# Kernel optimization log

Measured on AMD Instinct MI355X. Metric: run time of the kernel, lower is better.

## Reference

```python
import jax, jax.numpy as jnp
import numpy as np

E = 8          # num_local_experts
D = 1024       # hidden_size
F = 4096       # intermediate_size_moe
T = 2048       # tokens (seq_len)
K = 2          # num_experts_per_tok


def setup_inputs() -> dict:
    key = jax.random.key(0)
    k_x, k_r, k_g, k_u, k_d = jax.random.split(key, 5)
    s = lambda fan_in: 1.0 / np.sqrt(fan_in)
    return {
        "x_TD": jax.random.normal(k_x, (T, D), dtype=jnp.float32),
        "w_router_DE": jax.random.normal(k_r, (D, E), dtype=jnp.float32) * s(D),
        "kernel_gating_EDF": jax.random.normal(k_g, (E, D, F), dtype=jnp.float32) * s(D),
        "kernel_up_proj_EDF": jax.random.normal(k_u, (E, D, F), dtype=jnp.float32) * s(D),
        "kernel_down_proj_EFD": jax.random.normal(k_d, (E, F, D), dtype=jnp.float32) * s(F),
    }


def reference(x_TD, w_router_DE, kernel_gating_EDF, kernel_up_proj_EDF, kernel_down_proj_EFD):
    # --- Router: softmax -> top-k -> renormalize ---
    logits_TE = x_TD @ w_router_DE                       # [T, E]
    probs_TE = jax.nn.softmax(logits_TE, axis=-1)
    topk_vals, topk_idx = jax.lax.top_k(probs_TE, K)     # [T, K]
    topk_vals = topk_vals / jnp.sum(topk_vals, axis=-1, keepdims=True)  # renormalize=True
    # Dense combine weights: scatter top-k weights back to [T, E]
    weights_TE = jnp.sum(
        jax.nn.one_hot(topk_idx, E, dtype=x_TD.dtype) * topk_vals[..., None], axis=1
    )

    # --- Dense-mat expert MLP (SwiGLU), all experts for all tokens ---
    gate_TEF = jnp.einsum("td,edf->tef", x_TD, kernel_gating_EDF)
    up_TEF = jnp.einsum("td,edf->tef", x_TD, kernel_up_proj_EDF)
    h_TEF = jax.nn.silu(gate_TEF) * up_TEF

    # Down-project each expert and combine weighted by router
    # (apply_expert_weight_before_computation=False -> weight applied at combine)
    out_TD = jnp.einsum("tef,efd,te->td", h_TEF, kernel_down_proj_EFD, weights_TE)
    return out_TD
```

## Files before the change

### kernel.cpp

```cpp
#include <hip/hip_runtime.h>
#include <hip/hip_bf16.h>
#include <math.h>

#define T_TOK 2048
#define D_DIM 1024
#define F_DIM 4096
#define E_NUM 8
#define MAX_TILES 48

typedef __attribute__((ext_vector_type(8))) short short8;
typedef __attribute__((ext_vector_type(4))) short short4v;
typedef __attribute__((ext_vector_type(4))) float floatx4;

__device__ __forceinline__ short f2bf(float f) {
  union { float f; unsigned u; } v; v.f = f;
  unsigned r = v.u + 0x7fffu + ((v.u >> 16) & 1u);
  return (short)(r >> 16);
}

__device__ __forceinline__ void gld_lds16(const void* g, void* l) {
  __builtin_amdgcn_global_load_lds(
      (const __attribute__((address_space(1))) unsigned int*)g,
      (__attribute__((address_space(3))) unsigned int*)l, 16, 0, 0);
}

__global__ __launch_bounds__(256) void router_kernel(
    const float* __restrict__ x, const float* __restrict__ wr,
    int* __restrict__ counts, int* __restrict__ slot_sid, float* __restrict__ slot_w) {
  int lane = threadIdx.x & 63;
  int wave = threadIdx.x >> 6;
  int t = blockIdx.x * 4 + wave;
  const float* xr = x + (size_t)t * D_DIM;
  float acc[8];
#pragma unroll
  for (int e = 0; e < 8; e++) acc[e] = 0.f;
#pragma unroll
  for (int i = 0; i < 16; i++) {
    int d = i * 64 + lane;
    float xv = xr[d];
    const float* w = wr + d * 8;
    float4 w0 = *(const float4*)(w);
    float4 w1 = *(const float4*)(w + 4);
    acc[0] += xv * w0.x; acc[1] += xv * w0.y;
    acc[2] += xv * w0.z; acc[3] += xv * w0.w;
    acc[4] += xv * w1.x; acc[5] += xv * w1.y;
    acc[6] += xv * w1.z; acc[7] += xv * w1.w;
  }
#pragma unroll
  for (int off = 32; off > 0; off >>= 1) {
#pragma unroll
    for (int e = 0; e < 8; e++) acc[e] += __shfl_xor(acc[e], off, 64);
  }
  if (lane == 0) {
    int e1 = 0; float l1 = acc[0];
#pragma unroll
    for (int e = 1; e < 8; e++) { if (acc[e] > l1) { l1 = acc[e]; e1 = e; } }
    int e2 = -1; float l2 = -3.4e38f;
#pragma unroll
    for (int e = 0; e < 8; e++) { if (e != e1 && acc[e] > l2) { l2 = acc[e]; e2 = e; } }
    float w1 = 1.f / (1.f + __expf(l2 - l1));
    float w2 = 1.f - w1;
    int p1 = atomicAdd(&counts[e1], 1);
    slot_sid[e1 * T_TOK + p1] = 2 * t;
    slot_w[e1 * T_TOK + p1] = w1;
    int p2 = atomicAdd(&counts[e2], 1);
    slot_sid[e2 * T_TOK + p2] = 2 * t + 1;
    slot_w[e2 * T_TOK + p2] = w2;
  }
}

__global__ __launch_bounds__(64) void schedule_kernel(
    const int* __restrict__ counts, int* __restrict__ tiles) {
  if (threadIdx.x == 0) {
    int n = 0;
    for (int e = 0; e < E_NUM; e++) {
      int nt_ = (counts[e] + 127) >> 7;
      for (int m = 0; m < nt_; m++) tiles[n++] = (e << 8) | m;
    }
    for (int i = n; i < MAX_TILES; i++) tiles[i] = -1;
  }
}

__global__ __launch_bounds__(256) void cvt_x_kernel(const float* __restrict__ x,
                                                    short* __restrict__ Xb) {
  int i = blockIdx.x * 256 + threadIdx.x;
  float4 v = ((const float4*)x)[i];
  short4v s;
  s[0] = f2bf(v.x); s[1] = f2bf(v.y); s[2] = f2bf(v.z); s[3] = f2bf(v.w);
  ((short4v*)Xb)[i] = s;
}

__global__ __launch_bounds__(256) void transpose_cvt_kernel(
    const float* __restrict__ src, short* __restrict__ dst, int R, int C) {
  __shared__ short tileT[64 * 128];
  int cb = blockIdx.x * 64, rb = blockIdx.y * 128;
  size_t plane = (size_t)blockIdx.z * R * C;
  src += plane; dst += plane;
  int tid = threadIdx.x;
  int r0 = tid >> 4, c4 = (tid & 15) * 4;
#pragma unroll
  for (int i = 0; i < 8; i++) {
    int r = r0 + i * 16;
    float4 v = *(const float4*)&src[(size_t)(rb + r) * C + cb + c4];
    int rhw = ((r >> 3) << 3);
    int rlo = r & 7;
    tileT[(c4 + 0) * 128 + (((r >> 3) ^ ((c4 + 0) & 15)) << 3) + rlo] = f2bf(v.x);
    tileT[(c4 + 1) * 128 + (((r >> 3) ^ ((c4 + 1) & 15)) << 3) + rlo] = f2bf(v.y);
    tileT[(c4 + 2) * 128 + (((r >> 3) ^ ((c4 + 2) & 15)) << 3) + rlo] = f2bf(v.z);
    tileT[(c4 + 3) * 128 + (((r >> 3) ^ ((c4 + 3) & 15)) << 3) + rlo] = f2bf(v.w);
    (void)rhw;
  }
  __syncthreads();
  int c0 = tid >> 4, rq = tid & 15;
#pragma unroll
  for (int i = 0; i < 4; i++) {
    int c = c0 + i * 16;
    short8 s = *(const short8*)&tileT[c * 128 + ((rq ^ (c & 15)) << 3)];
    *(short8*)&dst[(size_t)(cb + c) * R + rb + rq * 8] = s;
  }
}

__global__ __launch_bounds__(256, 4) void gateup_kernel(
    const short* __restrict__ Xb, const short* __restrict__ WgT, const short* __restrict__ WuT,
    const int* __restrict__ counts, const int* __restrict__ slot_sid,
    const int* __restrict__ tiles, short* __restrict__ H) {
  __shared__ short smem[8192];
  __shared__ int s_sid[128];

  int bid = blockIdx.x;
  int tile = tiles[bid >> 6];
  if (tile < 0) return;
  int e  = tile >> 8;
  int mt = tile & 255;
  int nt = bid & 63;
  int n_e = counts[e];

  int tid = threadIdx.x;
  if (tid < 128) {
    int i = mt * 128 + tid;
    if (i > n_e - 1) i = n_e - 1;
    s_sid[tid] = slot_sid[e * T_TOK + i];
  }
  __syncthreads();

  int lane = tid & 63;
  int w = tid >> 6;
  int wm = w >> 1, wn = w & 1;
  int r16 = lane & 15, q = lane >> 4;

  int rl = lane >> 2;
  int kc = (lane & 3) * 8;
  const short* aP0 = Xb + (size_t)(s_sid[w * 16 + rl] >> 1) * D_DIM + kc;
  const short* aP1 = Xb + (size_t)(s_sid[64 + w * 16 + rl] >> 1) * D_DIM + kc;
  size_t wbase = (size_t)e * F_DIM * D_DIM + (size_t)(nt * 64 + w * 16 + rl) * D_DIM;
  const short* gP = WgT + wbase + kc;
  const short* uP = WuT + wbase + kc;
  short* ldsA0 = smem + w * 512;
  short* ldsA1 = smem + 2048 + w * 512;
  short* ldsBg = smem + 4096 + w * 512;
  short* ldsBu = smem + 6144 + w * 512;

  floatx4 zero4 = {0.f, 0.f, 0.f, 0.f};
  floatx4 accg[4][2], accu[4][2];
#pragma unroll
  for (int a = 0; a < 4; a++)
#pragma unroll
    for (int b = 0; b < 2; b++) { accg[a][b] = zero4; accu[a][b] = zero4; }

  for (int kb = 0; kb < D_DIM / 32; kb++) {
    gld_lds16(aP0, ldsA0);
    gld_lds16(aP1, ldsA1);
    gld_lds16(gP, ldsBg);
    gld_lds16(uP, ldsBu);
    aP0 += 32; aP1 += 32; gP += 32; uP += 32;
    __syncthreads();
    const short* As = smem;
    const short* Bg = smem + 4096;
    const short* Bu = smem + 6144;
    short8 af[4], bgf[2], buf_[2];
#pragma unroll
    for (int f = 0; f < 4; f++)
      af[f] = *(const short8*)&As[(wm * 64 + f * 16 + r16) * 32 + q * 8];
#pragma unroll
    for (int f = 0; f < 2; f++) {
      bgf[f]  = *(const short8*)&Bg[(wn * 32 + f * 16 + r16) * 32 + q * 8];
      buf_[f] = *(const short8*)&Bu[(wn * 32 + f * 16 + r16) * 32 + q * 8];
    }
#pragma unroll
    for (int fm = 0; fm < 4; fm++)
#pragma unroll
      for (int fn = 0; fn < 2; fn++) {
        accg[fm][fn] = __builtin_amdgcn_mfma_f32_16x16x32_bf16(af[fm], bgf[fn],  accg[fm][fn], 0, 0, 0);
        accu[fm][fn] = __builtin_amdgcn_mfma_f32_16x16x32_bf16(af[fm], buf_[fn], accu[fm][fn], 0, 0, 0);
      }
    __syncthreads();
  }

  short* slab = smem;
#pragma unroll
  for (int fm = 0; fm < 4; fm++) {
#pragma unroll
    for (int reg = 0; reg < 4; reg++) {
      int rowl = wm * 16 + q * 4 + reg;
#pragma unroll
      for (int fn = 0; fn < 2; fn++) {
        float g = accg[fm][fn][reg];
        float u = accu[fm][fn][reg];
        float h = g * u / (1.f + __expf(-g));
        slab[rowl * 72 + wn * 32 + fn * 16 + r16] = f2bf(h);
      }
    }
    __syncthreads();
    int rr = tid >> 3, cs = (tid & 7) * 8;
    int grow = (rr >> 4) * 64 + fm * 16 + (rr & 15);
    if (mt * 128 + grow < n_e) {
      int sid = s_sid[grow];
      short8 v0 = *(const short8*)&slab[rr * 72 + cs];
      *(short8*)(H + (size_t)sid * F_DIM + nt * 64 + cs) = v0;
    }
    __syncthreads();
  }
}

__global__ __launch_bounds__(256, 4) void down_kernel(
    const short* __restrict__ H, const short* __restrict__ WdT,
    const int* __restrict__ counts, const int* __restrict__ slot_sid,
    const float* __restrict__ slot_w, const int* __restrict__ tiles,
    float* __restrict__ Y) {
  __shared__ short smem[6144];
  __shared__ int s_sid[128];
  __shared__ float s_w[128];

  int bid = blockIdx.x;
  int tile = tiles[bid >> 6];
  if (tile < 0) return;
  int e  = tile >> 8;
  int mt = tile & 255;
  int sk = (bid >> 4) & 3;
  int nt = bid & 15;
  int n_e = counts[e];

  int tid = threadIdx.x;
  if (tid < 128) {
    int i = mt * 128 + tid;
    if (i > n_e - 1) i = n_e - 1;
    s_sid[tid] = slot_sid[e * T_TOK + i];
    s_w[tid]   = slot_w[e * T_TOK + i];
  }
  __syncthreads();

  int lane = tid & 63;
  int w = tid >> 6;
  int wm = w >> 1, wn = w & 1;
  int r16 = lane & 15, q = lane >> 4;

  int rl = lane >> 2;
  int kc = (lane & 3) * 8;
  int ks = sk * (F_DIM / 4);
  const short* aP0 = H + (size_t)s_sid[w * 16 + rl] * F_DIM + ks + kc;
  const short* aP1 = H + (size_t)s_sid[64 + w * 16 + rl] * F_DIM + ks + kc;
  const short* bP = WdT + ((size_t)e * D_DIM + nt * 64 + w * 16 + rl) * F_DIM + ks + kc;
  short* ldsA0 = smem + w * 512;
  short* ldsA1 = smem + 2048 + w * 512;
  short* ldsB  = smem + 4096 + w * 512;

  floatx4 zero4 = {0.f, 0.f, 0.f, 0.f};
  floatx4 acc[4][2];
#pragma unroll
  for (int a = 0; a < 4; a++)
#pragma unroll
    for (int b = 0; b < 2; b++) acc[a][b] = zero4;

  for (int kb = 0; kb < (F_DIM / 4) / 32; kb++) {
    gld_lds16(aP0, ldsA0);
    gld_lds16(aP1, ldsA1);
    gld_lds16(bP, ldsB);
    aP0 += 32; aP1 += 32; bP += 32;
    __syncthreads();
    const short* As = smem;
    const short* Bs = smem + 4096;
    short8 af[4], bf[2];
#pragma unroll
    for (int f = 0; f < 4; f++)
      af[f] = *(const short8*)&As[(wm * 64 + f * 16 + r16) * 32 + q * 8];
#pragma unroll
    for (int f = 0; f < 2; f++)
      bf[f] = *(const short8*)&Bs[(wn * 32 + f * 16 + r16) * 32 + q * 8];
#pragma unroll
    for (int fm = 0; fm < 4; fm++)
#pragma unroll
      for (int fn = 0; fn < 2; fn++)
        acc[fm][fn] = __builtin_amdgcn_mfma_f32_16x16x32_bf16(af[fm], bf[fn], acc[fm][fn], 0, 0, 0);
    __syncthreads();
  }

#pragma unroll
  for (int fm = 0; fm < 4; fm++) {
#pragma unroll
    for (int reg = 0; reg < 4; reg++) {
      int row = wm * 64 + fm * 16 + q * 4 + reg;
      int i = mt * 128 + row;
      if (i < n_e) {
        int sid = s_sid[row];
        float wgt = s_w[row];
        float* yp = Y + ((size_t)sk * (T_TOK * 2) + sid) * D_DIM + nt * 64 + wn * 32 + r16;
#pragma unroll
        for (int fn = 0; fn < 2; fn++)
          yp[fn * 16] = acc[fm][fn][reg] * wgt;
      }
    }
  }
}

__global__ __launch_bounds__(256) void combine_kernel(
    const float* __restrict__ Y, float* __restrict__ out) {
  int idx = blockIdx.x * 256 + threadIdx.x;
  int t = idx >> 8;
  int j = idx & 255;
  const floatx4* Yv = (const floatx4*)Y;
  floatx4 s = {0.f, 0.f, 0.f, 0.f};
#pragma unroll
  for (int sk = 0; sk < 4; sk++) {
    s += Yv[((size_t)sk * (T_TOK * 2) + 2 * t) * 256 + j];
    s += Yv[((size_t)sk * (T_TOK * 2) + 2 * t + 1) * 256 + j];
  }
  ((floatx4*)out)[idx] = s;
}

extern "C" void kernel_launch(void* const* d_in, const int* in_sizes, int n_in,
                              void* d_out, int out_size, void* d_ws, size_t ws_size,
                              hipStream_t stream) {
  const float* x  = (const float*)d_in[0];
  const float* wr = (const float*)d_in[1];
  const float* Wg = (const float*)d_in[2];
  const float* Wu = (const float*)d_in[3];
  const float* Wd = (const float*)d_in[4];
  float* out = (float*)d_out;

  char* ws = (char*)d_ws;
  int*   counts   = (int*)(ws);
  int*   tiles    = (int*)(ws + 2048);
  int*   slot_sid = (int*)(ws + 4096);
  float* slot_w   = (float*)(ws + 4096 + 65536);
  short* Xb       = (short*)(ws + 0x40000);
  short* H        = (short*)(ws + 0x800000);
  short* WgT      = (short*)(ws + 0x2800000);
  short* WuT      = (short*)(ws + 0x6800000);
  short* WdT      = WgT;
  float* Y4       = (float*)WuT;

  hipMemsetAsync(counts, 0, E_NUM * sizeof(int), stream);
  router_kernel<<<T_TOK / 4, 256, 0, stream>>>(x, wr, counts, slot_sid, slot_w);
  schedule_kernel<<<1, 64, 0, stream>>>(counts, tiles);
  cvt_x_kernel<<<T_TOK * D_DIM / 4 / 256, 256, 0, stream>>>(x, Xb);
  transpose_cvt_kernel<<<dim3(F_DIM / 64, D_DIM / 128, E_NUM), 256, 0, stream>>>(Wg, WgT, D_DIM, F_DIM);
  transpose_cvt_kernel<<<dim3(F_DIM / 64, D_DIM / 128, E_NUM), 256, 0, stream>>>(Wu, WuT, D_DIM, F_DIM);
  gateup_kernel<<<MAX_TILES * 64, 256, 0, stream>>>(Xb, WgT, WuT, counts, slot_sid, tiles, H);
  transpose_cvt_kernel<<<dim3(D_DIM / 64, F_DIM / 128, E_NUM), 256, 0, stream>>>(Wd, WdT, F_DIM, D_DIM);
  down_kernel<<<MAX_TILES * 64, 256, 0, stream>>>(H, WdT, counts, slot_sid, slot_w, tiles, Y4);
  combine_kernel<<<T_TOK * D_DIM / 4 / 256, 256, 0, stream>>>(Y4, out);
}
```

Baseline: 643.8 us.

## Fuse schedule into cvt_x, merge gate/up transposes, atomically combine down output

The schedule kernel is folded into the x conversion kernel, which now also computes per-expert prefix offsets. The gate and up weight transposes become one launch. H is now stored in expert-sorted contiguous order, so down-kernel A loads stream contiguous rows instead of gathered ones. The split-K partial buffer and combine kernel are replaced by float atomicAdd into a zeroed output. This removes launches and a large intermediate write/read, at the cost of atomic contention and nondeterministic summation order.

```diff
diff --git a/kernel.cpp b/kernel.cpp
--- a/kernel.cpp
+++ b/kernel.cpp
@@ -69,20 +69,18 @@
   }
 }
 
-__global__ __launch_bounds__(64) void schedule_kernel(
-    const int* __restrict__ counts, int* __restrict__ tiles) {
-  if (threadIdx.x == 0) {
-    int n = 0;
+__global__ __launch_bounds__(256) void cvt_x_kernel(
+    const float* __restrict__ x, short* __restrict__ Xb,
+    const int* __restrict__ counts, int* __restrict__ tiles, int* __restrict__ prefix) {
+  if (blockIdx.x == 0 && threadIdx.x == 0) {
+    int n = 0, p = 0;
     for (int e = 0; e < E_NUM; e++) {
+      prefix[e] = p; p += counts[e];
       int nt_ = (counts[e] + 127) >> 7;
       for (int m = 0; m < nt_; m++) tiles[n++] = (e << 8) | m;
     }
     for (int i = n; i < MAX_TILES; i++) tiles[i] = -1;
   }
-}
-
-__global__ __launch_bounds__(256) void cvt_x_kernel(const float* __restrict__ x,
-                                                    short* __restrict__ Xb) {
   int i = blockIdx.x * 256 + threadIdx.x;
   float4 v = ((const float4*)x)[i];
   short4v s;
@@ -90,25 +88,22 @@
   ((short4v*)Xb)[i] = s;
 }
 
-__global__ __launch_bounds__(256) void transpose_cvt_kernel(
-    const float* __restrict__ src, short* __restrict__ dst, int R, int C) {
+__device__ __forceinline__ void transpose_plane(
+    const float* __restrict__ src, short* __restrict__ dst, int R, int C,
+    int bx, int by) {
   __shared__ short tileT[64 * 128];
-  int cb = blockIdx.x * 64, rb = blockIdx.y * 128;
-  size_t plane = (size_t)blockIdx.z * R * C;
-  src += plane; dst += plane;
+  int cb = bx * 64, rb = by * 128;
   int tid = threadIdx.x;
   int r0 = tid >> 4, c4 = (tid & 15) * 4;
 #pragma unroll
   for (int i = 0; i < 8; i++) {
     int r = r0 + i * 16;
     float4 v = *(const float4*)&src[(size_t)(rb + r) * C + cb + c4];
-    int rhw = ((r >> 3) << 3);
     int rlo = r & 7;
     tileT[(c4 + 0) * 128 + (((r >> 3) ^ ((c4 + 0) & 15)) << 3) + rlo] = f2bf(v.x);
     tileT[(c4 + 1) * 128 + (((r >> 3) ^ ((c4 + 1) & 15)) << 3) + rlo] = f2bf(v.y);
     tileT[(c4 + 2) * 128 + (((r >> 3) ^ ((c4 + 2) & 15)) << 3) + rlo] = f2bf(v.z);
     tileT[(c4 + 3) * 128 + (((r >> 3) ^ ((c4 + 3) & 15)) << 3) + rlo] = f2bf(v.w);
-    (void)rhw;
   }
   __syncthreads();
   int c0 = tid >> 4, rq = tid & 15;
@@ -120,10 +115,27 @@
   }
 }
 
+__global__ __launch_bounds__(256) void transpose_cvt_kernel(
+    const float* __restrict__ src, short* __restrict__ dst, int R, int C) {
+  size_t plane = (size_t)blockIdx.z * R * C;
+  transpose_plane(src + plane, dst + plane, R, C, blockIdx.x, blockIdx.y);
+}
+
+__global__ __launch_bounds__(256) void transpose_cvt2_kernel(
+    const float* __restrict__ srcG, const float* __restrict__ srcU,
+    short* __restrict__ dstG, short* __restrict__ dstU, int R, int C) {
+  int z = blockIdx.z;
+  const float* src; short* dst;
+  if (z < E_NUM) { size_t p = (size_t)z * R * C; src = srcG + p; dst = dstG + p; }
+  else           { size_t p = (size_t)(z - E_NUM) * R * C; src = srcU + p; dst = dstU + p; }
+  transpose_plane(src, dst, R, C, blockIdx.x, blockIdx.y);
+}
+
 __global__ __launch_bounds__(256, 4) void gateup_kernel(
     const short* __restrict__ Xb, const short* __restrict__ WgT, const short* __restrict__ WuT,
     const int* __restrict__ counts, const int* __restrict__ slot_sid,
-    const int* __restrict__ tiles, short* __restrict__ H) {
+    const int* __restrict__ tiles, const int* __restrict__ prefix,
+    short* __restrict__ H) {
   __shared__ short smem[8192];
   __shared__ int s_sid[128];
 
@@ -134,6 +146,7 @@
   int mt = tile & 255;
   int nt = bid & 63;
   int n_e = counts[e];
+  int hbase = prefix[e] + mt * 128;
 
   int tid = threadIdx.x;
   if (tid < 128) {
@@ -214,9 +227,8 @@
     int rr = tid >> 3, cs = (tid & 7) * 8;
     int grow = (rr >> 4) * 64 + fm * 16 + (rr & 15);
     if (mt * 128 + grow < n_e) {
-      int sid = s_sid[grow];
       short8 v0 = *(const short8*)&slab[rr * 72 + cs];
-      *(short8*)(H + (size_t)sid * F_DIM + nt * 64 + cs) = v0;
+      *(short8*)(H + (size_t)(hbase + grow) * F_DIM + nt * 64 + cs) = v0;
     }
     __syncthreads();
   }
@@ -226,7 +238,7 @@
     const short* __restrict__ H, const short* __restrict__ WdT,
     const int* __restrict__ counts, const int* __restrict__ slot_sid,
     const float* __restrict__ slot_w, const int* __restrict__ tiles,
-    float* __restrict__ Y) {
+    const int* __restrict__ prefix, float* __restrict__ out) {
   __shared__ short smem[6144];
   __shared__ int s_sid[128];
   __shared__ float s_w[128];
@@ -239,6 +251,7 @@
   int sk = (bid >> 4) & 3;
   int nt = bid & 15;
   int n_e = counts[e];
+  int hbase = prefix[e] + mt * 128;
 
   int tid = threadIdx.x;
   if (tid < 128) {
@@ -257,8 +270,8 @@
   int rl = lane >> 2;
   int kc = (lane & 3) * 8;
   int ks = sk * (F_DIM / 4);
-  const short* aP0 = H + (size_t)s_sid[w * 16 + rl] * F_DIM + ks + kc;
-  const short* aP1 = H + (size_t)s_sid[64 + w * 16 + rl] * F_DIM + ks + kc;
+  const short* aP0 = H + (size_t)(hbase + w * 16 + rl) * F_DIM + ks + kc;
+  const short* aP1 = H + (size_t)(hbase + 64 + w * 16 + rl) * F_DIM + ks + kc;
   const short* bP = WdT + ((size_t)e * D_DIM + nt * 64 + w * 16 + rl) * F_DIM + ks + kc;
   short* ldsA0 = smem + w * 512;
   short* ldsA1 = smem + 2048 + w * 512;
@@ -301,30 +314,15 @@
       int row = wm * 64 + fm * 16 + q * 4 + reg;
       int i = mt * 128 + row;
       if (i < n_e) {
-        int sid = s_sid[row];
+        int t = s_sid[row] >> 1;
         float wgt = s_w[row];
-        float* yp = Y + ((size_t)sk * (T_TOK * 2) + sid) * D_DIM + nt * 64 + wn * 32 + r16;
+        float* yp = out + (size_t)t * D_DIM + nt * 64 + wn * 32 + r16;
 #pragma unroll
         for (int fn = 0; fn < 2; fn++)
-          yp[fn * 16] = acc[fm][fn][reg] * wgt;
+          atomicAdd(&yp[fn * 16], acc[fm][fn][reg] * wgt);
       }
     }
   }
-}
-
-__global__ __launch_bounds__(256) void combine_kernel(
-    const float* __restrict__ Y, float* __restrict__ out) {
-  int idx = blockIdx.x * 256 + threadIdx.x;
-  int t = idx >> 8;
-  int j = idx & 255;
-  const floatx4* Yv = (const floatx4*)Y;
-  floatx4 s = {0.f, 0.f, 0.f, 0.f};
-#pragma unroll
-  for (int sk = 0; sk < 4; sk++) {
-    s += Yv[((size_t)sk * (T_TOK * 2) + 2 * t) * 256 + j];
-    s += Yv[((size_t)sk * (T_TOK * 2) + 2 * t + 1) * 256 + j];
-  }
-  ((floatx4*)out)[idx] = s;
 }
 
 extern "C" void kernel_launch(void* const* d_in, const int* in_sizes, int n_in,
@@ -340,6 +338,7 @@
   char* ws = (char*)d_ws;
   int*   counts   = (int*)(ws);
   int*   tiles    = (int*)(ws + 2048);
+  int*   prefix   = (int*)(ws + 2048 + 512);
   int*   slot_sid = (int*)(ws + 4096);
   float* slot_w   = (float*)(ws + 4096 + 65536);
   short* Xb       = (short*)(ws + 0x40000);
@@ -347,16 +346,14 @@
   short* WgT      = (short*)(ws + 0x2800000);
   short* WuT      = (short*)(ws + 0x6800000);
   short* WdT      = WgT;
-  float* Y4       = (float*)WuT;
 
   hipMemsetAsync(counts, 0, E_NUM * sizeof(int), stream);
+  hipMemsetAsync(out, 0, (size_t)T_TOK * D_DIM * sizeof(float), stream);
   router_kernel<<<T_TOK / 4, 256, 0, stream>>>(x, wr, counts, slot_sid, slot_w);
-  schedule_kernel<<<1, 64, 0, stream>>>(counts, tiles);
-  cvt_x_kernel<<<T_TOK * D_DIM / 4 / 256, 256, 0, stream>>>(x, Xb);
-  transpose_cvt_kernel<<<dim3(F_DIM / 64, D_DIM / 128, E_NUM), 256, 0, stream>>>(Wg, WgT, D_DIM, F_DIM);
-  transpose_cvt_kernel<<<dim3(F_DIM / 64, D_DIM / 128, E_NUM), 256, 0, stream>>>(Wu, WuT, D_DIM, F_DIM);
-  gateup_kernel<<<MAX_TILES * 64, 256, 0, stream>>>(Xb, WgT, WuT, counts, slot_sid, tiles, H);
+  cvt_x_kernel<<<T_TOK * D_DIM / 4 / 256, 256, 0, stream>>>(x, Xb, counts, tiles, prefix);
+  transpose_cvt2_kernel<<<dim3(F_DIM / 64, D_DIM / 128, 2 * E_NUM), 256, 0, stream>>>(
+      Wg, Wu, WgT, WuT, D_DIM, F_DIM);
+  gateup_kernel<<<MAX_TILES * 64, 256, 0, stream>>>(Xb, WgT, WuT, counts, slot_sid, tiles, prefix, H);
   transpose_cvt_kernel<<<dim3(D_DIM / 64, F_DIM / 128, E_NUM), 256, 0, stream>>>(Wd, WdT, F_DIM, D_DIM);
-  down_kernel<<<MAX_TILES * 64, 256, 0, stream>>>(H, WdT, counts, slot_sid, slot_w, tiles, Y4);
-  combine_kernel<<<T_TOK * D_DIM / 4 / 256, 256, 0, stream>>>(Y4, out);
-}
+  down_kernel<<<MAX_TILES * 64, 256, 0, stream>>>(H, WdT, counts, slot_sid, slot_w, tiles, prefix, out);
+}
```

Measured after the change: 650.6 us. Within noise of the previous version (+1.0%).
